# Performance work log

Hardware: AMD Instinct MI355X
Metric: run time of the kernel (lower is better)

The kernel has to match this reference:

```python
import jax, jax.numpy as jnp
import numpy as np

B, C, R = 1024, 256, 7          # batch, channels, ROI feature map res
PATCH, DIL = 16, 2              # correlation patch size, dilation_patch
REP = 1024                      # representation_size
FLAT = PATCH * PATCH * R * R    # 12544 = fc1 input dim


def setup_inputs() -> dict:
    key = jax.random.key(0)
    k = jax.random.split(key, 8)
    return {
        "patch1": jax.random.normal(k[0], (B, C, R, R), dtype=jnp.float32),
        "patch2": jax.random.normal(k[1], (B, C, R, R), dtype=jnp.float32),
        "W1": jax.random.normal(k[2], (REP, FLAT), dtype=jnp.float32) * 0.01,
        "b1": jnp.zeros((REP,), dtype=jnp.float32),
        "W2": jax.random.normal(k[3], (REP, REP), dtype=jnp.float32) * 0.02,
        "b2": jnp.zeros((REP,), dtype=jnp.float32),
        "W3": jax.random.normal(k[4], (4, REP), dtype=jnp.float32) * 0.02,
        "b3": jnp.zeros((4,), dtype=jnp.float32),
    }


def _correlate(p1, p2):
    """SpatialCorrelationSampler(patch_size=16, dilation_patch=2), kernel=1, stride=1.
    out[b, pi, pj, i, j] = sum_c p1[b,c,i,j] * p2[b,c, i+(pi-8)*2, j+(pj-8)*2]
    (zero outside bounds). Returns [B, PATCH*PATCH, R, R]."""
    pad = (PATCH // 2) * DIL  # 16; displacements span [-16, 14]
    p2p = jnp.pad(p2, ((0, 0), (0, 0), (pad, pad), (pad, pad)))  # [B,C,39,39]
    outs = []
    for pi in range(PATCH):
        for pj in range(PATCH):
            # shifted window: row offset (pi-8)*2 + pad = 2*pi, same for cols
            win = p2p[:, :, DIL * pi:DIL * pi + R, DIL * pj:DIL * pj + R]
            outs.append(jnp.einsum('bchw,bchw->bhw', p1, win))
    return jnp.stack(outs, axis=1)  # [B, 256, 7, 7] -> matches torch flatten order


def reference(patch1, patch2, W1, b1, W2, b2, W3, b3):
    x = _correlate(patch1, patch2).reshape(patch1.shape[0], -1)  # [B, 12544]
    x = jax.nn.relu(x @ W1.T + b1)
    x = jax.nn.relu(x @ W2.T + b2)
    pred_boxes = x @ W3.T + b3  # [B, 4]
    return pred_boxes
```

## Files before the change

kernel.cpp:

```cpp
#include <hip/hip_runtime.h>

#define BATCH 1024
#define RR    49
#define SP    12544
#define KVALID 625
#define KPAD   640
#define REP_N  1024

typedef __attribute__((ext_vector_type(4))) float f32x4;
typedef __attribute__((ext_vector_type(8))) short s16x8;

__device__ __forceinline__ unsigned short f2bf_rne(float f) {
    unsigned int u = __float_as_uint(f);
    unsigned int r = u + 0x7FFFu + ((u >> 16) & 1u);
    return (unsigned short)(r >> 16);
}
__device__ __forceinline__ float bf2f(unsigned short h) {
    return __uint_as_float(((unsigned int)h) << 16);
}
__device__ __forceinline__ void split2(float v, unsigned short& h, unsigned short& l) {
    h = f2bf_rne(v);
    l = f2bf_rne(v - bf2f(h));
}
__device__ __forceinline__ unsigned int cvtpk_bf16(float a, float b) {
    unsigned int r;
    asm("v_cvt_pk_bf16_f32 %0, %1, %2" : "=v"(r) : "v"(a), "v"(b));
    return r;
}
__device__ __forceinline__ void cvt8(const float* v, s16x8& hv, s16x8& lv) {
    unsigned int* hp = (unsigned int*)&hv;
    unsigned int* lp = (unsigned int*)&lv;
    #pragma unroll
    for (int i = 0; i < 4; ++i) {
        float v0 = v[2 * i], v1 = v[2 * i + 1];
        unsigned int ph = cvtpk_bf16(v0, v1);
        float h0 = __uint_as_float(ph << 16);
        float h1 = __uint_as_float(ph & 0xFFFF0000u);
        unsigned int pl = cvtpk_bf16(v0 - h0, v1 - h1);
        hp[i] = ph; lp[i] = pl;
    }
}

__device__ __forceinline__ void dec25(int u, int& i, int& d) {
    int ii = (u >= 4) + (u >= 7) + (u >= 11) + (u >= 14) + (u >= 18) + (u >= 21);
    int cum = (7 * ii + 1) >> 1;
    i = ii;
    d = 2 * (u - cum) + (ii & 1);
}
__device__ __forceinline__ int enc25(int i, int d) {
    return ((7 * i + 1) >> 1) + ((d - (i & 1)) >> 1);
}

__device__ __forceinline__ int kflat_of(int a) {
    int ar = a / 25, ac = a % 25;
    int i, dy, j, dx;
    dec25(ar, i, dy);
    dec25(ac, j, dx);
    int pi = (dy + 16 - i) >> 1;
    int pj = (dx + 16 - j) >> 1;
    return (pi * 16 + pj) * 49 + i * 7 + j;
}

#define MM(d, a, b) d = __builtin_amdgcn_mfma_f32_16x16x32_bf16(a, b, d, 0, 0, 0)

__global__ __launch_bounds__(256) void corr_parity_kernel(
    const float* __restrict__ p1, const float* __restrict__ p2,
    unsigned short* __restrict__ xh, unsigned short* __restrict__ xl)
{
    __shared__ float4 Tb[2][2][832];
    __shared__ unsigned short SXh[KPAD];
    __shared__ unsigned short SXl[KPAD];

    const int b = blockIdx.x;
    const int t = threadIdx.x;
    const float* P1 = p1 + (size_t)b * SP;
    const float* P2 = p2 + (size_t)b * SP;

    const int wv   = t >> 6;
    const int lane = t & 63;
    const int fr   = lane & 15;
    const int fg   = (lane >> 4) * 8;

    const int ci = wv >> 1, cj = wv & 1;
    const int nj = 4 - cj;
    const int clsN = (4 - ci) * nj;
    const int pr = (fr < clsN) ? fr : 0;
    const int sPos = (2 * (pr / nj) + ci) * 7 + (2 * (pr % nj) + cj);

    const float* PS = (wv < 2) ? P1 : P2;
    const int tens  = wv >> 1;
    const int start = (wv & 1) * 7;
    const int nb    = (wv & 1) ? 6 : 7;

    #define STAGE(buf, chunk)                                                  \
        do {                                                                   \
            const int cOff_ = (chunk) * 3136;                                  \
            float4* T_ = &Tb[(buf)][tens][0];                                  \
            _Pragma("unroll")                                                  \
            for (int j_ = 0; j_ < 7; ++j_) {                                   \
                if (j_ < nb) {                                                 \
                    const int bq_  = start + j_;                               \
                    const int src_ = min(bq_ * 64 + lane, 783);                \
                    __builtin_amdgcn_global_load_lds(                          \
                        (const __attribute__((address_space(1))) unsigned int*)\
                            (PS + cOff_ + src_ * 4),                           \
                        (__attribute__((address_space(3))) unsigned int*)      \
                            (T_ + bq_ * 64),                                   \
                        16, 0, 0);                                             \
                }                                                              \
            }                                                                  \
        } while (0)

    for (int i = t; i < KPAD; i += 256) { SXh[i] = 0; SXl[i] = 0; }

    STAGE(0, 0);

    f32x4 acc = {};
    int cur = 0;
    for (int cc = 0; cc < 4; ++cc) {
        __syncthreads();
        if (cc < 3) STAGE(cur ^ 1, cc + 1);

        const float* Tf1 = (const float*)&Tb[cur][0][0];
        const float* Tf2 = (const float*)&Tb[cur][1][0];
        #pragma unroll
        for (int ks = 0; ks < 2; ++ks) {
            const int kb = (ks * 32 + fg) * RR + sPos;
            float av[8], bv[8];
            #pragma unroll
            for (int i = 0; i < 8; ++i) {
                av[i] = Tf1[kb + i * RR];
                bv[i] = Tf2[kb + i * RR];
            }
            s16x8 ah, al, bh, bl;
            cvt8(av, ah, al);
            cvt8(bv, bh, bl);
            MM(acc, ah, bh);
            MM(acc, ah, bl);
            MM(acc, al, bh);
        }
        cur ^= 1;
    }
    #undef STAGE

    const int arow = (lane >> 4) * 4;
    if (fr < clsN) {
        const int dy = 2 * (fr / nj) + ci;
        const int dx = 2 * (fr % nj) + cj;
        #pragma unroll
        for (int r = 0; r < 4; ++r) {
            const int rowp = arow + r;
            if (rowp < clsN) {
                const int i1 = 2 * (rowp / nj) + ci;
                const int j1 = 2 * (rowp % nj) + cj;
                const int aidx = enc25(i1, dy) * 25 + enc25(j1, dx);
                unsigned short hh, ll;
                split2(acc[r], hh, ll);
                SXh[aidx] = hh; SXl[aidx] = ll;
            }
        }
    }
    __syncthreads();

    unsigned int* rh = (unsigned int*)(xh + (size_t)b * KPAD);
    unsigned int* rl = (unsigned int*)(xl + (size_t)b * KPAD);
    const unsigned int* sh = (const unsigned int*)SXh;
    const unsigned int* sl = (const unsigned int*)SXl;
    for (int i = t; i < KPAD / 2; i += 256) { rh[i] = sh[i]; rl[i] = sl[i]; }
}

__global__ __launch_bounds__(256) void prep_weights_kernel(
    const float* __restrict__ W1, const float* __restrict__ W2,
    unsigned short* __restrict__ w1h, unsigned short* __restrict__ w1l,
    unsigned short* __restrict__ w2h, unsigned short* __restrict__ w2l)
{
    const int bid = blockIdx.x;
    if (bid < 2560) {
        int idx = bid * 256 + threadIdx.x;
        int n = idx / KPAD, a = idx - n * KPAD;
        float v = 0.f;
        if (a < KVALID) v = W1[(size_t)n * SP + kflat_of(a)];
        unsigned short h, l;
        split2(v, h, l);
        w1h[idx] = h; w1l[idx] = l;
    } else {
        int idx = ((bid - 2560) * 256 + threadIdx.x) * 4;
        float4 v = *(const float4*)&W2[idx];
        unsigned short h0, l0, h1, l1, h2, l2, h3, l3;
        split2(v.x, h0, l0); split2(v.y, h1, l1);
        split2(v.z, h2, l2); split2(v.w, h3, l3);
        *(ushort4*)&w2h[idx] = make_ushort4(h0, h1, h2, h3);
        *(ushort4*)&w2l[idx] = make_ushort4(l0, l1, l2, l3);
    }
}

template<bool SPLIT_OUT>
__global__ __launch_bounds__(256) void gemm_mfma(
    const unsigned short* __restrict__ Xh, const unsigned short* __restrict__ Xl, int ldx,
    const unsigned short* __restrict__ Wh, const unsigned short* __restrict__ Wl, int ldw,
    const float* __restrict__ bias, int K,
    float* __restrict__ Yf, unsigned short* __restrict__ Yh, unsigned short* __restrict__ Yl,
    int ldy)
{
    __shared__ unsigned short As[2][64][72];
    __shared__ unsigned short Bs[2][64][72];

    const int t = threadIdx.x;
    const int m_base = blockIdx.y * 64;
    const int n_base = blockIdx.x * 64;

    const int trow = t >> 2;
    const int tc   = (t & 3) * 8;

    const unsigned short* xh_p = Xh + (size_t)(m_base + trow) * ldx + tc;
    const unsigned short* xl_p = Xl + (size_t)(m_base + trow) * ldx + tc;
    const unsigned short* wh_p = Wh + (size_t)(n_base + trow) * ldw + tc;
    const unsigned short* wl_p = Wl + (size_t)(n_base + trow) * ldw + tc;

    const int wv   = t >> 6;
    const int lane = t & 63;
    const int wr = (wv >> 1) * 32;
    const int wc = (wv & 1) * 32;
    const int fr = lane & 15;
    const int fg = (lane >> 4) * 8;

    f32x4 acc00 = {}, acc01 = {}, acc10 = {}, acc11 = {};

    for (int k0 = 0; k0 < K; k0 += 64) {
        s16x8 vxh0 = *(const s16x8*)(xh_p + k0);
        s16x8 vxh1 = *(const s16x8*)(xh_p + k0 + 32);
        s16x8 vxl0 = *(const s16x8*)(xl_p + k0);
        s16x8 vxl1 = *(const s16x8*)(xl_p + k0 + 32);
        s16x8 vwh0 = *(const s16x8*)(wh_p + k0);
        s16x8 vwh1 = *(const s16x8*)(wh_p + k0 + 32);
        s16x8 vwl0 = *(const s16x8*)(wl_p + k0);
        s16x8 vwl1 = *(const s16x8*)(wl_p + k0 + 32);
        __syncthreads();
        *(s16x8*)&As[0][trow][tc]      = vxh0;
        *(s16x8*)&As[0][trow][tc + 32] = vxh1;
        *(s16x8*)&As[1][trow][tc]      = vxl0;
        *(s16x8*)&As[1][trow][tc + 32] = vxl1;
        *(s16x8*)&Bs[0][trow][tc]      = vwh0;
        *(s16x8*)&Bs[0][trow][tc + 32] = vwh1;
        *(s16x8*)&Bs[1][trow][tc]      = vwl0;
        *(s16x8*)&Bs[1][trow][tc + 32] = vwl1;
        __syncthreads();

        #pragma unroll
        for (int ks = 0; ks < 2; ++ks) {
            const int ko = ks * 32 + fg;
            s16x8 ah0 = *(const s16x8*)&As[0][wr + fr][ko];
            s16x8 ah1 = *(const s16x8*)&As[0][wr + 16 + fr][ko];
            s16x8 al0 = *(const s16x8*)&As[1][wr + fr][ko];
            s16x8 al1 = *(const s16x8*)&As[1][wr + 16 + fr][ko];
            s16x8 bh0 = *(const s16x8*)&Bs[0][wc + fr][ko];
            s16x8 bh1 = *(const s16x8*)&Bs[0][wc + 16 + fr][ko];
            s16x8 bl0 = *(const s16x8*)&Bs[1][wc + fr][ko];
            s16x8 bl1 = *(const s16x8*)&Bs[1][wc + 16 + fr][ko];

            MM(acc00, ah0, bh0); MM(acc00, ah0, bl0); MM(acc00, al0, bh0);
            MM(acc01, ah0, bh1); MM(acc01, ah0, bl1); MM(acc01, al0, bh1);
            MM(acc10, ah1, bh0); MM(acc10, ah1, bl0); MM(acc10, al1, bh0);
            MM(acc11, ah1, bh1); MM(acc11, ah1, bl1); MM(acc11, al1, bh1);
        }
    }

    const int arow = (lane >> 4) * 4;
    #pragma unroll
    for (int nf = 0; nf < 2; ++nf) {
        const int col = n_base + wc + nf * 16 + fr;
        const float bv = bias[col];
        #pragma unroll
        for (int mf = 0; mf < 2; ++mf) {
            const f32x4 a = (nf == 0) ? (mf == 0 ? acc00 : acc10)
                                      : (mf == 0 ? acc01 : acc11);
            #pragma unroll
            for (int r = 0; r < 4; ++r) {
                const int row = m_base + wr + mf * 16 + arow + r;
                float v = fmaxf(a[r] + bv, 0.f);
                if (SPLIT_OUT) {
                    unsigned short h, l;
                    split2(v, h, l);
                    Yh[(size_t)row * ldy + col] = h;
                    Yl[(size_t)row * ldy + col] = l;
                } else {
                    Yf[(size_t)row * ldy + col] = v;
                }
            }
        }
    }
}

__global__ __launch_bounds__(256) void head_kernel(
    const float* __restrict__ h2, const float* __restrict__ W3,
    const float* __restrict__ b3, float* __restrict__ out)
{
    const int b = blockIdx.x;
    const int t = threadIdx.x;
    const float* row = h2 + (size_t)b * REP_N;

    float a0 = 0.f, a1 = 0.f, a2 = 0.f, a3 = 0.f;
    for (int k = t; k < REP_N; k += 256) {
        float x = row[k];
        a0 = fmaf(x, W3[k],             a0);
        a1 = fmaf(x, W3[REP_N + k],     a1);
        a2 = fmaf(x, W3[2 * REP_N + k], a2);
        a3 = fmaf(x, W3[3 * REP_N + k], a3);
    }
    #pragma unroll
    for (int off = 32; off > 0; off >>= 1) {
        a0 += __shfl_down(a0, off);
        a1 += __shfl_down(a1, off);
        a2 += __shfl_down(a2, off);
        a3 += __shfl_down(a3, off);
    }
    __shared__ float red[4][4];
    int wid = t >> 6, lane = t & 63;
    if (lane == 0) { red[wid][0] = a0; red[wid][1] = a1; red[wid][2] = a2; red[wid][3] = a3; }
    __syncthreads();
    if (t < 4) {
        out[b * 4 + t] = red[0][t] + red[1][t] + red[2][t] + red[3][t] + b3[t];
    }
}

extern "C" void kernel_launch(void* const* d_in, const int* in_sizes, int n_in,
                              void* d_out, int out_size, void* d_ws, size_t ws_size,
                              hipStream_t stream) {
    const float* p1 = (const float*)d_in[0];
    const float* p2 = (const float*)d_in[1];
    const float* W1 = (const float*)d_in[2];
    const float* b1 = (const float*)d_in[3];
    const float* W2 = (const float*)d_in[4];
    const float* b2 = (const float*)d_in[5];
    const float* W3 = (const float*)d_in[6];
    const float* b3 = (const float*)d_in[7];
    float* out = (float*)d_out;

    char* ws = (char*)d_ws;
    unsigned short* xh  = (unsigned short*)(ws + 0);
    unsigned short* xl  = (unsigned short*)(ws + 1310720);
    unsigned short* w1h = (unsigned short*)(ws + 2621440);
    unsigned short* w1l = (unsigned short*)(ws + 3932160);
    float*          h2  = (float*)(ws + 0);
    unsigned short* h1h = (unsigned short*)(ws + 5242880);
    unsigned short* h1l = (unsigned short*)(ws + 7340032);
    unsigned short* w2h = (unsigned short*)(ws + 9437184);
    unsigned short* w2l = (unsigned short*)(ws + 11534336);

    corr_parity_kernel<<<BATCH, 256, 0, stream>>>(p1, p2, xh, xl);
    prep_weights_kernel<<<3584, 256, 0, stream>>>(W1, W2, w1h, w1l, w2h, w2l);

    gemm_mfma<true><<<dim3(16, 16), 256, 0, stream>>>(
        xh, xl, KPAD, w1h, w1l, KPAD, b1, KPAD,
        (float*)nullptr, h1h, h1l, REP_N);

    gemm_mfma<false><<<dim3(16, 16), 256, 0, stream>>>(
        h1h, h1l, REP_N, w2h, w2l, REP_N, b2, REP_N,
        h2, (unsigned short*)nullptr, (unsigned short*)nullptr, REP_N);

    head_kernel<<<BATCH, 256, 0, stream>>>(h2, W3, b3, out);
}
```

Baseline: 64.52 us.

## Fuse correlation and weight prep kernels, halve GEMM N-tile, finer corr staging

Merges the correlation and weight-preparation kernels into one launch, interleaving correlation blocks with weight-split blocks so the two independent jobs share the GPU. The correlation kernel now stages half-size channel chunks (8 stages of 32 channels), which cuts LDS per block and may allow more blocks per CU. The GEMMs switch from 64x64 to 64x32 tiles, doubling the grid to 512 blocks to fill more CUs, at the cost of more A-tile reloads and fewer MFMAs per LDS load.

```diff
diff --git a/kernel.cpp b/kernel.cpp
--- a/kernel.cpp
+++ b/kernel.cpp
@@ -63,18 +63,52 @@
 
 #define MM(d, a, b) d = __builtin_amdgcn_mfma_f32_16x16x32_bf16(a, b, d, 0, 0, 0)
 
-__global__ __launch_bounds__(256) void corr_parity_kernel(
+__global__ __launch_bounds__(256) void corr_prep_kernel(
     const float* __restrict__ p1, const float* __restrict__ p2,
-    unsigned short* __restrict__ xh, unsigned short* __restrict__ xl)
+    const float* __restrict__ W1, const float* __restrict__ W2,
+    unsigned short* __restrict__ xh, unsigned short* __restrict__ xl,
+    unsigned short* __restrict__ w1h, unsigned short* __restrict__ w1l,
+    unsigned short* __restrict__ w2h, unsigned short* __restrict__ w2l)
 {
-    __shared__ float4 Tb[2][2][832];
+    __shared__ float4 Tb[2][2][448];
     __shared__ unsigned short SXh[KPAD];
     __shared__ unsigned short SXl[KPAD];
 
-    const int b = blockIdx.x;
-    const int t = threadIdx.x;
-    const float* P1 = p1 + (size_t)b * SP;
-    const float* P2 = p2 + (size_t)b * SP;
+    const int bid = blockIdx.x;
+    const int t   = threadIdx.x;
+
+    bool isCorr = false;
+    int cid = 0, pid = 0;
+    if (bid < 2048) {
+        if ((bid & 1) == 0) { isCorr = true; cid = bid >> 1; }
+        else                { pid = bid >> 1; }
+    } else {
+        pid = 1024 + (bid - 2048);
+    }
+
+    if (!isCorr) {
+        if (pid < 2560) {
+            int idx = pid * 256 + t;
+            int n = idx / KPAD, a = idx - n * KPAD;
+            float v = 0.f;
+            if (a < KVALID) v = W1[(size_t)n * SP + kflat_of(a)];
+            unsigned short h, l;
+            split2(v, h, l);
+            w1h[idx] = h; w1l[idx] = l;
+        } else {
+            int idx = ((pid - 2560) * 256 + t) * 4;
+            float4 v = *(const float4*)&W2[idx];
+            unsigned short h0, l0, h1, l1, h2, l2, h3, l3;
+            split2(v.x, h0, l0); split2(v.y, h1, l1);
+            split2(v.z, h2, l2); split2(v.w, h3, l3);
+            *(ushort4*)&w2h[idx] = make_ushort4(h0, h1, h2, h3);
+            *(ushort4*)&w2l[idx] = make_ushort4(l0, l1, l2, l3);
+        }
+        return;
+    }
+
+    const float* P1 = p1 + (size_t)cid * SP;
+    const float* P2 = p2 + (size_t)cid * SP;
 
     const int wv   = t >> 6;
     const int lane = t & 63;
@@ -89,21 +123,21 @@
 
     const float* PS = (wv < 2) ? P1 : P2;
     const int tens  = wv >> 1;
-    const int start = (wv & 1) * 7;
-    const int nb    = (wv & 1) ? 6 : 7;
-
-    #define STAGE(buf, chunk)                                                  \
+    const int start = (wv & 1) * 4;
+    const int nb    = (wv & 1) ? 3 : 4;
+
+    #define STAGE(buf, hc)                                                     \
         do {                                                                   \
-            const int cOff_ = (chunk) * 3136;                                  \
+            const int off_ = (hc) * 1568;                                      \
             float4* T_ = &Tb[(buf)][tens][0];                                  \
             _Pragma("unroll")                                                  \
-            for (int j_ = 0; j_ < 7; ++j_) {                                   \
+            for (int j_ = 0; j_ < 4; ++j_) {                                   \
                 if (j_ < nb) {                                                 \
                     const int bq_  = start + j_;                               \
-                    const int src_ = min(bq_ * 64 + lane, 783);                \
+                    const int src_ = min(bq_ * 64 + lane, 391);                \
                     __builtin_amdgcn_global_load_lds(                          \
                         (const __attribute__((address_space(1))) unsigned int*)\
-                            (PS + cOff_ + src_ * 4),                           \
+                            (PS + off_ + src_ * 4),                            \
                         (__attribute__((address_space(3))) unsigned int*)      \
                             (T_ + bq_ * 64),                                   \
                         16, 0, 0);                                             \
@@ -117,28 +151,26 @@
 
     f32x4 acc = {};
     int cur = 0;
-    for (int cc = 0; cc < 4; ++cc) {
+    #pragma unroll
+    for (int hc = 0; hc < 8; ++hc) {
         __syncthreads();
-        if (cc < 3) STAGE(cur ^ 1, cc + 1);
+        if (hc < 7) STAGE(cur ^ 1, hc + 1);
 
         const float* Tf1 = (const float*)&Tb[cur][0][0];
         const float* Tf2 = (const float*)&Tb[cur][1][0];
+        const int kb = fg * RR + sPos;
+        float av[8], bv[8];
         #pragma unroll
-        for (int ks = 0; ks < 2; ++ks) {
-            const int kb = (ks * 32 + fg) * RR + sPos;
-            float av[8], bv[8];
-            #pragma unroll
-            for (int i = 0; i < 8; ++i) {
-                av[i] = Tf1[kb + i * RR];
-                bv[i] = Tf2[kb + i * RR];
-            }
-            s16x8 ah, al, bh, bl;
-            cvt8(av, ah, al);
-            cvt8(bv, bh, bl);
-            MM(acc, ah, bh);
-            MM(acc, ah, bl);
-            MM(acc, al, bh);
-        }
+        for (int i = 0; i < 8; ++i) {
+            av[i] = Tf1[kb + i * RR];
+            bv[i] = Tf2[kb + i * RR];
+        }
+        s16x8 ah, al, bh, bl;
+        cvt8(av, ah, al);
+        cvt8(bv, bh, bl);
+        MM(acc, ah, bh);
+        MM(acc, ah, bl);
+        MM(acc, al, bh);
         cur ^= 1;
     }
     #undef STAGE
@@ -162,36 +194,11 @@
     }
     __syncthreads();
 
-    unsigned int* rh = (unsigned int*)(xh + (size_t)b * KPAD);
-    unsigned int* rl = (unsigned int*)(xl + (size_t)b * KPAD);
+    unsigned int* rh = (unsigned int*)(xh + (size_t)cid * KPAD);
+    unsigned int* rl = (unsigned int*)(xl + (size_t)cid * KPAD);
     const unsigned int* sh = (const unsigned int*)SXh;
     const unsigned int* sl = (const unsigned int*)SXl;
     for (int i = t; i < KPAD / 2; i += 256) { rh[i] = sh[i]; rl[i] = sl[i]; }
-}
-
-__global__ __launch_bounds__(256) void prep_weights_kernel(
-    const float* __restrict__ W1, const float* __restrict__ W2,
-    unsigned short* __restrict__ w1h, unsigned short* __restrict__ w1l,
-    unsigned short* __restrict__ w2h, unsigned short* __restrict__ w2l)
-{
-    const int bid = blockIdx.x;
-    if (bid < 2560) {
-        int idx = bid * 256 + threadIdx.x;
-        int n = idx / KPAD, a = idx - n * KPAD;
-        float v = 0.f;
-        if (a < KVALID) v = W1[(size_t)n * SP + kflat_of(a)];
-        unsigned short h, l;
-        split2(v, h, l);
-        w1h[idx] = h; w1l[idx] = l;
-    } else {
-        int idx = ((bid - 2560) * 256 + threadIdx.x) * 4;
-        float4 v = *(const float4*)&W2[idx];
-        unsigned short h0, l0, h1, l1, h2, l2, h3, l3;
-        split2(v.x, h0, l0); split2(v.y, h1, l1);
-        split2(v.z, h2, l2); split2(v.w, h3, l3);
-        *(ushort4*)&w2h[idx] = make_ushort4(h0, h1, h2, h3);
-        *(ushort4*)&w2l[idx] = make_ushort4(l0, l1, l2, l3);
-    }
 }
 
 template<bool SPLIT_OUT>
@@ -203,47 +210,45 @@
     int ldy)
 {
     __shared__ unsigned short As[2][64][72];
-    __shared__ unsigned short Bs[2][64][72];
+    __shared__ unsigned short Bs[2][32][72];
 
     const int t = threadIdx.x;
     const int m_base = blockIdx.y * 64;
-    const int n_base = blockIdx.x * 64;
+    const int n_base = blockIdx.x * 32;
 
     const int trow = t >> 2;
     const int tc   = (t & 3) * 8;
+    const int trB  = t >> 3;
+    const int tcB  = (t & 7) * 8;
 
     const unsigned short* xh_p = Xh + (size_t)(m_base + trow) * ldx + tc;
     const unsigned short* xl_p = Xl + (size_t)(m_base + trow) * ldx + tc;
-    const unsigned short* wh_p = Wh + (size_t)(n_base + trow) * ldw + tc;
-    const unsigned short* wl_p = Wl + (size_t)(n_base + trow) * ldw + tc;
+    const unsigned short* wh_p = Wh + (size_t)(n_base + trB) * ldw + tcB;
+    const unsigned short* wl_p = Wl + (size_t)(n_base + trB) * ldw + tcB;
 
     const int wv   = t >> 6;
     const int lane = t & 63;
     const int wr = (wv >> 1) * 32;
-    const int wc = (wv & 1) * 32;
+    const int wc = (wv & 1) * 16;
     const int fr = lane & 15;
     const int fg = (lane >> 4) * 8;
 
-    f32x4 acc00 = {}, acc01 = {}, acc10 = {}, acc11 = {};
+    f32x4 acc0 = {}, acc1 = {};
 
     for (int k0 = 0; k0 < K; k0 += 64) {
         s16x8 vxh0 = *(const s16x8*)(xh_p + k0);
         s16x8 vxh1 = *(const s16x8*)(xh_p + k0 + 32);
         s16x8 vxl0 = *(const s16x8*)(xl_p + k0);
         s16x8 vxl1 = *(const s16x8*)(xl_p + k0 + 32);
-        s16x8 vwh0 = *(const s16x8*)(wh_p + k0);
-        s16x8 vwh1 = *(const s16x8*)(wh_p + k0 + 32);
-        s16x8 vwl0 = *(const s16x8*)(wl_p + k0);
-        s16x8 vwl1 = *(const s16x8*)(wl_p + k0 + 32);
+        s16x8 vwh  = *(const s16x8*)(wh_p + k0);
+        s16x8 vwl  = *(const s16x8*)(wl_p + k0);
         __syncthreads();
         *(s16x8*)&As[0][trow][tc]      = vxh0;
         *(s16x8*)&As[0][trow][tc + 32] = vxh1;
         *(s16x8*)&As[1][trow][tc]      = vxl0;
         *(s16x8*)&As[1][trow][tc + 32] = vxl1;
-        *(s16x8*)&Bs[0][trow][tc]      = vwh0;
-        *(s16x8*)&Bs[0][trow][tc + 32] = vwh1;
-        *(s16x8*)&Bs[1][trow][tc]      = vwl0;
-        *(s16x8*)&Bs[1][trow][tc + 32] = vwl1;
+        *(s16x8*)&Bs[0][trB][tcB]      = vwh;
+        *(s16x8*)&Bs[1][trB][tcB]      = vwl;
         __syncthreads();
 
         #pragma unroll
@@ -253,39 +258,31 @@
             s16x8 ah1 = *(const s16x8*)&As[0][wr + 16 + fr][ko];
             s16x8 al0 = *(const s16x8*)&As[1][wr + fr][ko];
             s16x8 al1 = *(const s16x8*)&As[1][wr + 16 + fr][ko];
-            s16x8 bh0 = *(const s16x8*)&Bs[0][wc + fr][ko];
-            s16x8 bh1 = *(const s16x8*)&Bs[0][wc + 16 + fr][ko];
-            s16x8 bl0 = *(const s16x8*)&Bs[1][wc + fr][ko];
-            s16x8 bl1 = *(const s16x8*)&Bs[1][wc + 16 + fr][ko];
-
-            MM(acc00, ah0, bh0); MM(acc00, ah0, bl0); MM(acc00, al0, bh0);
-            MM(acc01, ah0, bh1); MM(acc01, ah0, bl1); MM(acc01, al0, bh1);
-            MM(acc10, ah1, bh0); MM(acc10, ah1, bl0); MM(acc10, al1, bh0);
-            MM(acc11, ah1, bh1); MM(acc11, ah1, bl1); MM(acc11, al1, bh1);
+            s16x8 bh  = *(const s16x8*)&Bs[0][wc + fr][ko];
+            s16x8 bl  = *(const s16x8*)&Bs[1][wc + fr][ko];
+
+            MM(acc0, ah0, bh); MM(acc0, ah0, bl); MM(acc0, al0, bh);
+            MM(acc1, ah1, bh); MM(acc1, ah1, bl); MM(acc1, al1, bh);
         }
     }
 
     const int arow = (lane >> 4) * 4;
+    const int col = n_base + wc + fr;
+    const float bv = bias[col];
     #pragma unroll
-    for (int nf = 0; nf < 2; ++nf) {
-        const int col = n_base + wc + nf * 16 + fr;
-        const float bv = bias[col];
+    for (int mf = 0; mf < 2; ++mf) {
+        const f32x4 a = mf == 0 ? acc0 : acc1;
         #pragma unroll
-        for (int mf = 0; mf < 2; ++mf) {
-            const f32x4 a = (nf == 0) ? (mf == 0 ? acc00 : acc10)
-                                      : (mf == 0 ? acc01 : acc11);
-            #pragma unroll
-            for (int r = 0; r < 4; ++r) {
-                const int row = m_base + wr + mf * 16 + arow + r;
-                float v = fmaxf(a[r] + bv, 0.f);
-                if (SPLIT_OUT) {
-                    unsigned short h, l;
-                    split2(v, h, l);
-                    Yh[(size_t)row * ldy + col] = h;
-                    Yl[(size_t)row * ldy + col] = l;
-                } else {
-                    Yf[(size_t)row * ldy + col] = v;
-                }
+        for (int r = 0; r < 4; ++r) {
+            const int row = m_base + wr + mf * 16 + arow + r;
+            float v = fmaxf(a[r] + bv, 0.f);
+            if (SPLIT_OUT) {
+                unsigned short h, l;
+                split2(v, h, l);
+                Yh[(size_t)row * ldy + col] = h;
+                Yl[(size_t)row * ldy + col] = l;
+            } else {
+                Yf[(size_t)row * ldy + col] = v;
             }
         }
     }
@@ -347,14 +344,14 @@
     unsigned short* w2h = (unsigned short*)(ws + 9437184);
     unsigned short* w2l = (unsigned short*)(ws + 11534336);
 
-    corr_parity_kernel<<<BATCH, 256, 0, stream>>>(p1, p2, xh, xl);
-    prep_weights_kernel<<<3584, 256, 0, stream>>>(W1, W2, w1h, w1l, w2h, w2l);
-
-    gemm_mfma<true><<<dim3(16, 16), 256, 0, stream>>>(
+    corr_prep_kernel<<<4608, 256, 0, stream>>>(
+        p1, p2, W1, W2, xh, xl, w1h, w1l, w2h, w2l);
+
+    gemm_mfma<true><<<dim3(32, 16), 256, 0, stream>>>(
         xh, xl, KPAD, w1h, w1l, KPAD, b1, KPAD,
         (float*)nullptr, h1h, h1l, REP_N);
 
-    gemm_mfma<false><<<dim3(16, 16), 256, 0, stream>>>(
+    gemm_mfma<false><<<dim3(32, 16), 256, 0, stream>>>(
         h1h, h1l, REP_N, w2h, w2l, REP_N, b2, REP_N,
         h2, (unsigned short*)nullptr, (unsigned short*)nullptr, REP_N);
 
```

Result: faster. 62.59 us (-3.0%).
